# Kernel optimization log

Measured on AMD Instinct MI355X. Metric: run time of the kernel, lower is better.

## Reference

```python
import jax, jax.numpy as jnp
import numpy as np

NUM_LEVELS = 16
FEATURES_PER_LEVEL = 2
LOG2_HASHMAP_SIZE = 19
HASHMAP_SIZE = 2 ** LOG2_HASHMAP_SIZE
BASE_RES = 16
FINEST_RES = 512
B_GROWTH = np.exp((np.log(FINEST_RES) - np.log(BASE_RES)) / (NUM_LEVELS - 1))
# 8 trilinear corner offsets [8, 3]
OFFSETS = jnp.array([[dx, dy, dz] for dx in (0, 1) for dy in (0, 1) for dz in (0, 1)], dtype=jnp.int32)
PRIMES = jnp.array([1, 73856093, 19349663], dtype=jnp.int32)


def setup_inputs() -> dict:
    key = jax.random.key(0)
    k1, k2 = jax.random.split(key)
    positions = jax.random.uniform(k1, (16, 65536, 3), dtype=jnp.float32, minval=-1.0, maxval=1.0)
    tables = jax.random.normal(k2, (NUM_LEVELS, HASHMAP_SIZE, FEATURES_PER_LEVEL), dtype=jnp.float32) * 0.01
    return {"positions": positions, "tables": tables}


def _encode(positions, tables):
    pos = (positions + 1.0) * 0.5  # [B,S,3] in [0,1]
    outs = []
    for level in range(NUM_LEVELS):
        res = int(np.floor(BASE_RES * B_GROWTH ** level))
        scaled = pos * (res - 1)  # [B,S,3]
        base = jnp.floor(scaled).astype(jnp.int32)
        frac = scaled - base.astype(scaled.dtype)  # [B,S,3]
        corners = base[None] + OFFSETS[:, None, None, :]  # [8,B,S,3]
        # int32 wrapping overflow matches torch's .int() arithmetic; mod gives non-negative
        h = (corners * PRIMES).sum(-1, dtype=jnp.int32) % HASHMAP_SIZE  # [8,B,S]
        feats = tables[level][h]  # [8,B,S,F]
        w = jnp.where(OFFSETS[:, None, None, :] == 1, frac[None], 1.0 - frac[None]).prod(-1)  # [8,B,S]
        outs.append((feats * w[..., None]).sum(0))  # [B,S,F]
    return jnp.concatenate(outs, axis=-1)  # [B,S,L*F]


def reference(positions, tables):
    return _encode(positions, tables)
```

## Files before the change

kernel.cpp:

```cpp
#include <hip/hip_runtime.h>

#define NLEVELS 16
#define HSIZE (1u << 19)
#define HMASK ((1u << 19) - 1u)
#define P2 73856093u
#define P3 19349663u

typedef float nf4 __attribute__((ext_vector_type(4)));

__constant__ int c_res[NLEVELS] = {16, 20, 25, 32, 40, 50, 64, 80,
                                   101, 128, 161, 203, 256, 322, 406, 512};

template <bool TO_WS>
__global__ __launch_bounds__(256) void hashgrid_kernel(
    const float* __restrict__ positions,
    const float* __restrict__ tables,
    float2* __restrict__ dst,
    int npoints)
{
    int nch = (npoints + 255) >> 8;
    int b = blockIdx.x;
    int L, chunk;
    if (TO_WS) {
        int xcd = b & 7;
        int j = b >> 3;
        L = xcd + ((j >= nch) ? 8 : 0);
        chunk = (j >= nch) ? (j - nch) : j;
    } else {
        L = b / nch;
        chunk = b - L * nch;
    }
    int p = (chunk << 8) + threadIdx.x;
    if (p >= npoints) return;

    float px = (positions[3 * p + 0] + 1.0f) * 0.5f;
    float py = (positions[3 * p + 1] + 1.0f) * 0.5f;
    float pz = (positions[3 * p + 2] + 1.0f) * 0.5f;

    float rm1 = (float)(c_res[L] - 1);
    float sx = px * rm1, sy = py * rm1, sz = pz * rm1;
    float bx = floorf(sx), by = floorf(sy), bz = floorf(sz);
    float fx = sx - bx, fy = sy - by, fz = sz - bz;

    unsigned ix = (unsigned)(int)bx;
    unsigned iy = (unsigned)(int)by;
    unsigned iz = (unsigned)(int)bz;

    unsigned s00 = ix + iy * P2 + iz * P3;
    unsigned hl0 = s00 & HMASK;
    unsigned hl1 = (s00 + P2) & HMASK;
    unsigned hl2 = (s00 + P3) & HMASK;
    unsigned hl3 = (s00 + P2 + P3) & HMASK;

    const float* tabf = tables + (size_t)L * (2u * HSIZE);
    float2 t0 = ((const float2*)tabf)[0];

    unsigned w0 = (hl0 == HMASK) ? 1u : 0u;
    unsigned w1 = (hl1 == HMASK) ? 1u : 0u;
    unsigned w2 = (hl2 == HMASK) ? 1u : 0u;
    unsigned w3 = (hl3 == HMASK) ? 1u : 0u;

    nf4 g0 = *(const nf4*)(tabf + 2u * (hl0 - w0));
    nf4 g1 = *(const nf4*)(tabf + 2u * (hl1 - w1));
    nf4 g2 = *(const nf4*)(tabf + 2u * (hl2 - w2));
    nf4 g3 = *(const nf4*)(tabf + 2u * (hl3 - w3));

    float l0x = w0 ? g0.z : g0.x, l0y = w0 ? g0.w : g0.y;
    float h0x = w0 ? t0.x : g0.z, h0y = w0 ? t0.y : g0.w;
    float l1x = w1 ? g1.z : g1.x, l1y = w1 ? g1.w : g1.y;
    float h1x = w1 ? t0.x : g1.z, h1y = w1 ? t0.y : g1.w;
    float l2x = w2 ? g2.z : g2.x, l2y = w2 ? g2.w : g2.y;
    float h2x = w2 ? t0.x : g2.z, h2y = w2 ? t0.y : g2.w;
    float l3x = w3 ? g3.z : g3.x, l3y = w3 ? g3.w : g3.y;
    float h3x = w3 ? t0.x : g3.z, h3y = w3 ? t0.y : g3.w;

    float wx0 = 1.0f - fx, wy0 = 1.0f - fy, wz0 = 1.0f - fz;
    float c0 = wy0 * wz0;
    float c1 = fy * wz0;
    float c2 = wy0 * fz;
    float c3 = fy * fz;

    float o0 = c0 * (wx0 * l0x + fx * h0x)
             + c1 * (wx0 * l1x + fx * h1x)
             + c2 * (wx0 * l2x + fx * h2x)
             + c3 * (wx0 * l3x + fx * h3x);
    float o1 = c0 * (wx0 * l0y + fx * h0y)
             + c1 * (wx0 * l1y + fx * h1y)
             + c2 * (wx0 * l2y + fx * h2y)
             + c3 * (wx0 * l3y + fx * h3y);

    if (TO_WS) {
        dst[((size_t)chunk * NLEVELS + L) * 256 + threadIdx.x] = make_float2(o0, o1);
    } else {
        dst[(size_t)p * NLEVELS + L] = make_float2(o0, o1);
    }
}

__global__ __launch_bounds__(256) void transpose_kernel(
    const nf4* __restrict__ ws4,
    nf4* __restrict__ out4,
    int npoints)
{
    __shared__ float2 lds[256][NLEVELS + 1];
    int c = blockIdx.x;
    int t = threadIdx.x;
    size_t base = (size_t)c * 2048;

#pragma unroll
    for (int k = 0; k < 8; ++k) {
        int i = (k << 8) + t;
        nf4 v = ws4[base + i];
        int L = i >> 7;
        int m = i & 127;
        lds[m][L]       = make_float2(v.x, v.y);
        lds[m + 128][L] = make_float2(v.z, v.w);
    }
    __syncthreads();

#pragma unroll
    for (int k = 0; k < 8; ++k) {
        int i = (k << 8) + t;
        int pp = i >> 3;
        int q = i & 7;
        int r = (pp >> 1) | ((pp & 1) << 7);
        float2 a = lds[r][2 * q];
        float2 bb = lds[r][2 * q + 1];
        nf4 v = {a.x, a.y, bb.x, bb.y};
        __builtin_nontemporal_store(v, &out4[base + i]);
    }
}

extern "C" void kernel_launch(void* const* d_in, const int* in_sizes, int n_in,
                              void* d_out, int out_size, void* d_ws, size_t ws_size,
                              hipStream_t stream) {
    const float* positions = (const float*)d_in[0];
    const float* tables = (const float*)d_in[1];
    int npoints = in_sizes[0] / 3;
    int nch = (npoints + 255) >> 8;
    int blocks = NLEVELS * nch;

    size_t ws_needed = (size_t)NLEVELS * npoints * sizeof(float2);
    if (ws_size >= ws_needed && (npoints & 255) == 0) {
        float2* ws = (float2*)d_ws;
        hashgrid_kernel<true><<<blocks, 256, 0, stream>>>(positions, tables, ws, npoints);
        transpose_kernel<<<npoints / 256, 256, 0, stream>>>((const nf4*)ws,
                                                            (nf4*)d_out, npoints);
    } else {
        hashgrid_kernel<false><<<blocks, 256, 0, stream>>>(positions, tables,
                                                           (float2*)d_out, npoints);
    }
}
```

Before: 507.0 us.

## Fuse per-level hashgrid encoding and transpose into a single kernel

Replaces the two-kernel scheme (one block per level and chunk writing to a workspace, then a transpose kernel) with one kernel where each block handles 256 points across all 16 levels. Results are staged in LDS and written out as coalesced nontemporal vectors. This removes the workspace write and read round-trip, the second launch, and the repeated position loads. In exchange it drops the XCD-to-level mapping that kept each level's table within one L2. A rotated starting level per block only partly recovers that locality, so table gathers may see more L2 misses.

```diff
diff --git a/kernel.cpp b/kernel.cpp
--- a/kernel.cpp
+++ b/kernel.cpp
@@ -11,122 +11,99 @@
 __constant__ int c_res[NLEVELS] = {16, 20, 25, 32, 40, 50, 64, 80,
                                    101, 128, 161, 203, 256, 322, 406, 512};
 
-template <bool TO_WS>
-__global__ __launch_bounds__(256) void hashgrid_kernel(
+__global__ __launch_bounds__(256) void hashgrid_fused(
     const float* __restrict__ positions,
     const float* __restrict__ tables,
-    float2* __restrict__ dst,
-    int npoints)
-{
-    int nch = (npoints + 255) >> 8;
-    int b = blockIdx.x;
-    int L, chunk;
-    if (TO_WS) {
-        int xcd = b & 7;
-        int j = b >> 3;
-        L = xcd + ((j >= nch) ? 8 : 0);
-        chunk = (j >= nch) ? (j - nch) : j;
-    } else {
-        L = b / nch;
-        chunk = b - L * nch;
-    }
-    int p = (chunk << 8) + threadIdx.x;
-    if (p >= npoints) return;
-
-    float px = (positions[3 * p + 0] + 1.0f) * 0.5f;
-    float py = (positions[3 * p + 1] + 1.0f) * 0.5f;
-    float pz = (positions[3 * p + 2] + 1.0f) * 0.5f;
-
-    float rm1 = (float)(c_res[L] - 1);
-    float sx = px * rm1, sy = py * rm1, sz = pz * rm1;
-    float bx = floorf(sx), by = floorf(sy), bz = floorf(sz);
-    float fx = sx - bx, fy = sy - by, fz = sz - bz;
-
-    unsigned ix = (unsigned)(int)bx;
-    unsigned iy = (unsigned)(int)by;
-    unsigned iz = (unsigned)(int)bz;
-
-    unsigned s00 = ix + iy * P2 + iz * P3;
-    unsigned hl0 = s00 & HMASK;
-    unsigned hl1 = (s00 + P2) & HMASK;
-    unsigned hl2 = (s00 + P3) & HMASK;
-    unsigned hl3 = (s00 + P2 + P3) & HMASK;
-
-    const float* tabf = tables + (size_t)L * (2u * HSIZE);
-    float2 t0 = ((const float2*)tabf)[0];
-
-    unsigned w0 = (hl0 == HMASK) ? 1u : 0u;
-    unsigned w1 = (hl1 == HMASK) ? 1u : 0u;
-    unsigned w2 = (hl2 == HMASK) ? 1u : 0u;
-    unsigned w3 = (hl3 == HMASK) ? 1u : 0u;
-
-    nf4 g0 = *(const nf4*)(tabf + 2u * (hl0 - w0));
-    nf4 g1 = *(const nf4*)(tabf + 2u * (hl1 - w1));
-    nf4 g2 = *(const nf4*)(tabf + 2u * (hl2 - w2));
-    nf4 g3 = *(const nf4*)(tabf + 2u * (hl3 - w3));
-
-    float l0x = w0 ? g0.z : g0.x, l0y = w0 ? g0.w : g0.y;
-    float h0x = w0 ? t0.x : g0.z, h0y = w0 ? t0.y : g0.w;
-    float l1x = w1 ? g1.z : g1.x, l1y = w1 ? g1.w : g1.y;
-    float h1x = w1 ? t0.x : g1.z, h1y = w1 ? t0.y : g1.w;
-    float l2x = w2 ? g2.z : g2.x, l2y = w2 ? g2.w : g2.y;
-    float h2x = w2 ? t0.x : g2.z, h2y = w2 ? t0.y : g2.w;
-    float l3x = w3 ? g3.z : g3.x, l3y = w3 ? g3.w : g3.y;
-    float h3x = w3 ? t0.x : g3.z, h3y = w3 ? t0.y : g3.w;
-
-    float wx0 = 1.0f - fx, wy0 = 1.0f - fy, wz0 = 1.0f - fz;
-    float c0 = wy0 * wz0;
-    float c1 = fy * wz0;
-    float c2 = wy0 * fz;
-    float c3 = fy * fz;
-
-    float o0 = c0 * (wx0 * l0x + fx * h0x)
-             + c1 * (wx0 * l1x + fx * h1x)
-             + c2 * (wx0 * l2x + fx * h2x)
-             + c3 * (wx0 * l3x + fx * h3x);
-    float o1 = c0 * (wx0 * l0y + fx * h0y)
-             + c1 * (wx0 * l1y + fx * h1y)
-             + c2 * (wx0 * l2y + fx * h2y)
-             + c3 * (wx0 * l3y + fx * h3y);
-
-    if (TO_WS) {
-        dst[((size_t)chunk * NLEVELS + L) * 256 + threadIdx.x] = make_float2(o0, o1);
-    } else {
-        dst[(size_t)p * NLEVELS + L] = make_float2(o0, o1);
-    }
-}
-
-__global__ __launch_bounds__(256) void transpose_kernel(
-    const nf4* __restrict__ ws4,
     nf4* __restrict__ out4,
     int npoints)
 {
     __shared__ float2 lds[256][NLEVELS + 1];
-    int c = blockIdx.x;
-    int t = threadIdx.x;
-    size_t base = (size_t)c * 2048;
+    const int c = blockIdx.x;
+    const int t = threadIdx.x;
+    const int p = (c << 8) + t;
+    const bool valid = (p < npoints);
+
+    float px = 0.0f, py = 0.0f, pz = 0.0f;
+    if (valid) {
+        px = (positions[3 * p + 0] + 1.0f) * 0.5f;
+        py = (positions[3 * p + 1] + 1.0f) * 0.5f;
+        pz = (positions[3 * p + 2] + 1.0f) * 0.5f;
+    }
+
+    const int Lbase = (c & 7) << 1;
 
 #pragma unroll
-    for (int k = 0; k < 8; ++k) {
-        int i = (k << 8) + t;
-        nf4 v = ws4[base + i];
-        int L = i >> 7;
-        int m = i & 127;
-        lds[m][L]       = make_float2(v.x, v.y);
-        lds[m + 128][L] = make_float2(v.z, v.w);
+    for (int it = 0; it < NLEVELS; ++it) {
+        const int L = (Lbase + it) & (NLEVELS - 1);
+        const float rm1 = (float)(c_res[L] - 1);
+        float sx = px * rm1, sy = py * rm1, sz = pz * rm1;
+        float bx = floorf(sx), by = floorf(sy), bz = floorf(sz);
+        float fx = sx - bx, fy = sy - by, fz = sz - bz;
+
+        unsigned ix = (unsigned)(int)bx;
+        unsigned iy = (unsigned)(int)by;
+        unsigned iz = (unsigned)(int)bz;
+
+        unsigned s00 = ix + iy * P2 + iz * P3;
+        unsigned hl0 = s00 & HMASK;
+        unsigned hl1 = (s00 + P2) & HMASK;
+        unsigned hl2 = (s00 + P3) & HMASK;
+        unsigned hl3 = (s00 + P2 + P3) & HMASK;
+
+        const float* tabf = tables + (size_t)L * (2u * HSIZE);
+        float2 t0 = ((const float2*)tabf)[0];
+
+        unsigned w0 = (hl0 == HMASK) ? 1u : 0u;
+        unsigned w1 = (hl1 == HMASK) ? 1u : 0u;
+        unsigned w2 = (hl2 == HMASK) ? 1u : 0u;
+        unsigned w3 = (hl3 == HMASK) ? 1u : 0u;
+
+        nf4 g0 = *(const nf4*)(tabf + 2u * (hl0 - w0));
+        nf4 g1 = *(const nf4*)(tabf + 2u * (hl1 - w1));
+        nf4 g2 = *(const nf4*)(tabf + 2u * (hl2 - w2));
+        nf4 g3 = *(const nf4*)(tabf + 2u * (hl3 - w3));
+
+        float l0x = w0 ? g0.z : g0.x, l0y = w0 ? g0.w : g0.y;
+        float h0x = w0 ? t0.x : g0.z, h0y = w0 ? t0.y : g0.w;
+        float l1x = w1 ? g1.z : g1.x, l1y = w1 ? g1.w : g1.y;
+        float h1x = w1 ? t0.x : g1.z, h1y = w1 ? t0.y : g1.w;
+        float l2x = w2 ? g2.z : g2.x, l2y = w2 ? g2.w : g2.y;
+        float h2x = w2 ? t0.x : g2.z, h2y = w2 ? t0.y : g2.w;
+        float l3x = w3 ? g3.z : g3.x, l3y = w3 ? g3.w : g3.y;
+        float h3x = w3 ? t0.x : g3.z, h3y = w3 ? t0.y : g3.w;
+
+        float wx0 = 1.0f - fx, wy0 = 1.0f - fy, wz0 = 1.0f - fz;
+        float c0 = wy0 * wz0;
+        float c1 = fy * wz0;
+        float c2 = wy0 * fz;
+        float c3 = fy * fz;
+
+        float o0 = c0 * (wx0 * l0x + fx * h0x)
+                 + c1 * (wx0 * l1x + fx * h1x)
+                 + c2 * (wx0 * l2x + fx * h2x)
+                 + c3 * (wx0 * l3x + fx * h3x);
+        float o1 = c0 * (wx0 * l0y + fx * h0y)
+                 + c1 * (wx0 * l1y + fx * h1y)
+                 + c2 * (wx0 * l2y + fx * h2y)
+                 + c3 * (wx0 * l3y + fx * h3y);
+
+        lds[t][L] = make_float2(o0, o1);
     }
+
     __syncthreads();
 
+    const size_t base = (size_t)c * 2048;
 #pragma unroll
     for (int k = 0; k < 8; ++k) {
         int i = (k << 8) + t;
         int pp = i >> 3;
         int q = i & 7;
-        int r = (pp >> 1) | ((pp & 1) << 7);
-        float2 a = lds[r][2 * q];
-        float2 bb = lds[r][2 * q + 1];
-        nf4 v = {a.x, a.y, bb.x, bb.y};
-        __builtin_nontemporal_store(v, &out4[base + i]);
+        if ((c << 8) + pp < npoints) {
+            float2 a = lds[pp][2 * q];
+            float2 b = lds[pp][2 * q + 1];
+            nf4 v = {a.x, a.y, b.x, b.y};
+            __builtin_nontemporal_store(v, &out4[base + i]);
+        }
     }
 }
 
@@ -136,17 +113,7 @@
     const float* positions = (const float*)d_in[0];
     const float* tables = (const float*)d_in[1];
     int npoints = in_sizes[0] / 3;
-    int nch = (npoints + 255) >> 8;
-    int blocks = NLEVELS * nch;
-
-    size_t ws_needed = (size_t)NLEVELS * npoints * sizeof(float2);
-    if (ws_size >= ws_needed && (npoints & 255) == 0) {
-        float2* ws = (float2*)d_ws;
-        hashgrid_kernel<true><<<blocks, 256, 0, stream>>>(positions, tables, ws, npoints);
-        transpose_kernel<<<npoints / 256, 256, 0, stream>>>((const nf4*)ws,
-                                                            (nf4*)d_out, npoints);
-    } else {
-        hashgrid_kernel<false><<<blocks, 256, 0, stream>>>(positions, tables,
-                                                           (float2*)d_out, npoints);
-    }
+    int blocks = (npoints + 255) >> 8;
+    hashgrid_fused<<<blocks, 256, 0, stream>>>(positions, tables,
+                                               (nf4*)d_out, npoints);
 }
```

After: 809.2 us. 59.6% more time.
